# Performance work log

Hardware: AMD Instinct MI355X
Metric: run time of the kernel (lower is better)

Reference implementation:

```python
import jax, jax.numpy as jnp
import numpy as np

N = 50000      # num nodes
E = 600000     # num edges (avg degree 12)
IN = 256       # in_feats
H = 128        # h_feats
P = 2          # prop_step
LN_EPS = 1e-5


def setup_inputs() -> dict:
    key = jax.random.key(0)
    ks = jax.random.split(key, 8)
    return {
        "in_feat": jax.random.normal(ks[0], (N, IN), jnp.float32),
        "row": jax.random.randint(ks[1], (E,), 0, N),  # target node of each edge
        "col": jax.random.randint(ks[2], (E,), 0, N),  # source node of each edge
        "lin_w": jax.random.normal(ks[3], (H, IN), jnp.float32) / np.sqrt(IN).astype(np.float32),
        "lin_b": jnp.zeros((H,), jnp.float32),
        "conv_w": jax.random.normal(ks[4], (H, H), jnp.float32) / np.sqrt(H).astype(np.float32),
        "conv_b": jnp.zeros((H,), jnp.float32),
        "root_emb": jax.random.normal(ks[5], (1, H), jnp.float32) * 0.02,
        "ln_gamma": jnp.ones((P, H), jnp.float32),
        "ln_beta": jnp.zeros((P, H), jnp.float32),
    }


def _layernorm(x, g, b):
    mu = jnp.mean(x, axis=-1, keepdims=True)
    var = jnp.mean(jnp.square(x - mu), axis=-1, keepdims=True)
    return (x - mu) * jax.lax.rsqrt(var + LN_EPS) * g + b


def reference(in_feat, row, col, lin_w, lin_b, conv_w, conv_b, root_emb, ln_gamma, ln_beta):
    n = in_feat.shape[0]
    h = in_feat @ lin_w.T + lin_b                      # [N, H]

    # OGB-style degree norm with +1 trick (original edges, row = target)
    deg = jax.ops.segment_sum(jnp.ones_like(row, dtype=h.dtype), row, num_segments=n) + 1.0
    deg_inv = 1.0 / deg                                # deg >= 1, never inf

    # GCNConv symmetric norm with self loops: D^-1/2 (A+I) D^-1/2
    loop = jnp.arange(n)
    r2 = jnp.concatenate([row, loop])                  # [E+N] targets
    c2 = jnp.concatenate([col, loop])                  # [E+N] sources
    d2 = jax.ops.segment_sum(jnp.ones_like(r2, dtype=h.dtype), r2, num_segments=n)
    dis = jnp.where(d2 > 0, jax.lax.rsqrt(jnp.maximum(d2, 1.0)), 0.0)
    ew = dis[r2] * dis[c2]                             # [E+N] edge weights

    root = root_emb[0]                                 # [H]
    ori = h
    for i in range(P):
        if i != 0:
            h = h + ori                                # residual
            h = _layernorm(h, ln_gamma[i], ln_beta[i])
            h = jax.nn.relu(h)
            # dropout=0.0 -> identity
        xw = h @ conv_w.T                              # [N, H]
        h_msg = jax.ops.segment_sum(ew[:, None] * xw[c2], r2, num_segments=n) + conv_b
        root_contrib = jax.nn.relu(h + root) * deg_inv[:, None]
        h = h_msg + root_contrib
    return h
```

## Files before the change

### kernel.cpp

```cpp
#include <hip/hip_runtime.h>

#define NN 50000
#define EE 600000
#define INF 256
#define HF 128
#define CEB ((EE + 255) / 256)
#define GB ((NN + 63) / 64)
#define NBCH ((NN + 255) / 256)

typedef __attribute__((ext_vector_type(8))) short short8;
typedef __attribute__((ext_vector_type(4))) float floatx4;

__device__ __forceinline__ unsigned short f32_to_bf16_rne(float x) {
    unsigned int u = __float_as_uint(x);
    unsigned int r = (u + 0x7FFFu + ((u >> 16) & 1u)) >> 16;
    return (unsigned short)r;
}
__device__ __forceinline__ float bf16_to_f32(unsigned short h) {
    return __uint_as_float(((unsigned int)h) << 16);
}
__device__ __forceinline__ float bf16lo_u32(unsigned int u) {
    return __uint_as_float(u << 16);
}
__device__ __forceinline__ float bf16hi_u32(unsigned int u) {
    return __uint_as_float(u & 0xFFFF0000u);
}
__device__ __forceinline__ void cvt_hilo8(float4 v0, float4 v1, short8& hs, short8& ls) {
    float x[8] = {v0.x, v0.y, v0.z, v0.w, v1.x, v1.y, v1.z, v1.w};
    union { short8 s; unsigned short u[8]; } H, L;
#pragma unroll
    for (int k = 0; k < 8; ++k) {
        unsigned short hi = f32_to_bf16_rne(x[k]);
        H.u[k] = hi;
        L.u[k] = f32_to_bf16_rne(x[k] - bf16_to_f32(hi));
    }
    hs = H.s;
    ls = L.s;
}

__global__ void scan_phase1(const int* __restrict__ cnt, int* __restrict__ bsum, int n) {
    __shared__ int sdata[256];
    int t = threadIdx.x;
    int i = blockIdx.x * 256 + t;
    sdata[t] = (i < n) ? cnt[i] : 0;
    __syncthreads();
    for (int s = 128; s > 0; s >>= 1) {
        if (t < s) sdata[t] += sdata[t + s];
        __syncthreads();
    }
    if (t == 0) bsum[blockIdx.x] = sdata[0];
}

__global__ void scan_phase3(const int* __restrict__ cnt, const int* __restrict__ bsum,
                            int* __restrict__ row_start,
                            float* __restrict__ deg_inv, float* __restrict__ dis,
                            int n, int nb, int E) {
    __shared__ int sb[256];
    __shared__ int sdata[256];
    int t = threadIdx.x;
    sb[t] = (t < nb) ? bsum[t] : 0;
    __syncthreads();
    for (int s = 1; s < 256; s <<= 1) {
        int add = (t >= s) ? sb[t - s] : 0;
        __syncthreads();
        sb[t] += add;
        __syncthreads();
    }
    int base = sb[blockIdx.x] - bsum[blockIdx.x];
    int i = blockIdx.x * 256 + t;
    int v = (i < n) ? cnt[i] : 0;
    sdata[t] = v;
    __syncthreads();
    for (int s = 1; s < 256; s <<= 1) {
        int add = (t >= s) ? sdata[t - s] : 0;
        __syncthreads();
        sdata[t] += add;
        __syncthreads();
    }
    if (i < n) {
        row_start[i] = base + sdata[t] - v;
        float d = (float)(v + 1);
        deg_inv[i] = 1.0f / d;
        dis[i] = rsqrtf(d);
    }
    if (blockIdx.x == 0 && t == 0) row_start[n] = E;
}

__global__ void fill_csr(const int* __restrict__ row, const int* __restrict__ col,
                         const int* __restrict__ row_start, const int* __restrict__ pos,
                         int* __restrict__ csr_col, int E) {
    int e = blockIdx.x * blockDim.x + threadIdx.x;
    if (e < E) {
        int p = row_start[row[e]] + pos[e];
        __builtin_nontemporal_store(col[e], &csr_col[p]);
    }
}

template <int K, int MODE>
__device__ __forceinline__ void gemm_tile(
    int bidx,
    const float* __restrict__ Af,
    const unsigned short* __restrict__ Ahg, const unsigned short* __restrict__ Alg,
    const float* __restrict__ Wsrc,
    const float* __restrict__ bias,
    float* __restrict__ C, unsigned short* __restrict__ Cbf,
    const float* __restrict__ h, const float* __restrict__ deg_inv,
    const float* __restrict__ root,
    const float* __restrict__ gamma, const float* __restrict__ beta,
    unsigned short* WS, int M) {
    constexpr int NKC = K / 32;
    const int t = threadIdx.x;
    const int wave = t >> 6;
    const int lane = t & 63;
    const int lrow = lane & 15;
    const int quad = lane >> 4;
    const int bm = bidx * 64;
    int arow = bm + wave * 16 + lrow;
    if (arow >= M) arow = M - 1;

    floatx4 acc[8];
#pragma unroll
    for (int nt = 0; nt < 8; ++nt) acc[nt] = (floatx4){0.f, 0.f, 0.f, 0.f};

#pragma unroll
    for (int pp = 0; pp < NKC / 2; ++pp) {
        if (pp) __syncthreads();
#pragma unroll
        for (int u0 = 0; u0 < 4; ++u0) {
            int u = t + u0 * 256;
            int kc2 = u >> 9;
            int nt = (u >> 6) & 7;
            int ln = u & 63;
            int rw = nt * 16 + (ln & 15);
            int koff = (pp * 2 + kc2) * 32 + (ln >> 4) * 8;
            const float* p = &Wsrc[(size_t)rw * K + koff];
            float4 v0 = *reinterpret_cast<const float4*>(p);
            float4 v1 = *reinterpret_cast<const float4*>(p + 4);
            short8 hs, ls;
            cvt_hilo8(v0, v1, hs, ls);
            *reinterpret_cast<short8*>(&WS[kc2 * 8192 + nt * 512 + ln * 8]) = hs;
            *reinterpret_cast<short8*>(&WS[kc2 * 8192 + 4096 + nt * 512 + ln * 8]) = ls;
        }
        __syncthreads();
#pragma unroll
        for (int k2 = 0; k2 < 2; ++k2) {
            int kc = pp * 2 + k2;
            short8 afh, afl;
            if (MODE == 0) {
                const float* ap = &Af[(size_t)arow * K + kc * 32 + quad * 8];
                float4 a0 = *reinterpret_cast<const float4*>(ap);
                float4 a1 = *reinterpret_cast<const float4*>(ap + 4);
                cvt_hilo8(a0, a1, afh, afl);
            } else {
                size_t ao = (size_t)arow * K + kc * 32 + quad * 8;
                afh = *reinterpret_cast<const short8*>(&Ahg[ao]);
                afl = *reinterpret_cast<const short8*>(&Alg[ao]);
            }
            const unsigned short* wb = &WS[k2 * 8192 + lane * 8];
#pragma unroll
            for (int nt = 0; nt < 8; ++nt) {
                short8 bfh = *reinterpret_cast<const short8*>(wb + nt * 512);
                short8 bfl = *reinterpret_cast<const short8*>(wb + 4096 + nt * 512);
                acc[nt] = __builtin_amdgcn_mfma_f32_16x16x32_bf16(afh, bfh, acc[nt], 0, 0, 0);
                acc[nt] = __builtin_amdgcn_mfma_f32_16x16x32_bf16(afl, bfh, acc[nt], 0, 0, 0);
                acc[nt] = __builtin_amdgcn_mfma_f32_16x16x32_bf16(afh, bfl, acc[nt], 0, 0, 0);
            }
        }
    }

    float cb[8], rt[8], gm[8], bt[8];
#pragma unroll
    for (int nt = 0; nt < 8; ++nt) {
        int colh = nt * 16 + lrow;
        cb[nt] = bias[colh];
        if (MODE >= 1) rt[nt] = root[colh];
        if (MODE == 1) { gm[nt] = gamma[colh]; bt[nt] = beta[colh]; }
    }

#pragma unroll
    for (int r = 0; r < 4; ++r) {
        int grow = bm + wave * 16 + quad * 4 + r;
        bool ok = (grow < M);
        int gr = ok ? grow : M - 1;
        float x[8];
        if (MODE == 0) {
#pragma unroll
            for (int nt = 0; nt < 8; ++nt) x[nt] = acc[nt][r] + cb[nt];
        } else {
            float di = deg_inv[gr];
            float hv[8];
#pragma unroll
            for (int nt = 0; nt < 8; ++nt) hv[nt] = h[(size_t)gr * HF + nt * 16 + lrow];
#pragma unroll
            for (int nt = 0; nt < 8; ++nt) {
                float v = acc[nt][r] + cb[nt] + fmaxf(hv[nt] + rt[nt], 0.f) * di;
                x[nt] = (MODE == 1) ? v + hv[nt] : v;
            }
        }
        if (MODE == 1) {
            float s = 0.f;
#pragma unroll
            for (int nt = 0; nt < 8; ++nt) s += x[nt];
#pragma unroll
            for (int m = 1; m < 16; m <<= 1) s += __shfl_xor(s, m, 64);
            float mu = s * (1.0f / HF);
            float var = 0.f;
#pragma unroll
            for (int nt = 0; nt < 8; ++nt) { float d = x[nt] - mu; var += d * d; }
#pragma unroll
            for (int m = 1; m < 16; m <<= 1) var += __shfl_xor(var, m, 64);
            float rs = rsqrtf(var * (1.0f / HF) + 1e-5f);
            if (ok) {
#pragma unroll
                for (int nt = 0; nt < 8; ++nt) {
                    int colh = nt * 16 + lrow;
                    float y = fmaxf((x[nt] - mu) * rs * gm[nt] + bt[nt], 0.f);
                    C[(size_t)grow * HF + colh] = y;
                    Cbf[(size_t)grow * HF + colh] = f32_to_bf16_rne(y);
                }
            }
        } else if (MODE == 0) {
            if (ok) {
#pragma unroll
                for (int nt = 0; nt < 8; ++nt) {
                    int colh = nt * 16 + lrow;
                    C[(size_t)grow * HF + colh] = x[nt];
                    Cbf[(size_t)grow * HF + colh] = f32_to_bf16_rne(x[nt]);
                }
            }
        } else {
            if (ok) {
#pragma unroll
                for (int nt = 0; nt < 8; ++nt)
                    C[(size_t)grow * HF + nt * 16 + lrow] = x[nt];
            }
        }
    }
}

__global__ __launch_bounds__(256) void gemm0_count(
    const float* __restrict__ in_feat, const float* __restrict__ lin_w,
    const float* __restrict__ lin_b,
    float* __restrict__ h0, unsigned short* __restrict__ hbf,
    const int* __restrict__ row, int* __restrict__ cnt, int* __restrict__ pos) {
    __shared__ unsigned short WS[2 * 8192];
    int b = blockIdx.x;
    if (b < GB) {
        gemm_tile<INF, 0>(b, in_feat, nullptr, nullptr, lin_w, lin_b,
                          h0, hbf, nullptr, nullptr, nullptr,
                          nullptr, nullptr, WS, NN);
        return;
    }
    int e = (b - GB) * 256 + threadIdx.x;
    if (e < EE) pos[e] = atomicAdd(&cnt[row[e]], 1);
}

template <int MODE>
__global__ __launch_bounds__(256) void gemm_conv(
    const unsigned short* __restrict__ agg_hi, const unsigned short* __restrict__ agg_lo,
    const float* __restrict__ conv_w, const float* __restrict__ conv_b,
    float* __restrict__ C, unsigned short* __restrict__ Cbf,
    const float* __restrict__ h, const float* __restrict__ deg_inv,
    const float* __restrict__ root,
    const float* __restrict__ gamma, const float* __restrict__ beta) {
    __shared__ unsigned short WS[2 * 8192];
    gemm_tile<HF, MODE>(blockIdx.x, nullptr, agg_hi, agg_lo, conv_w, conv_b,
                        C, Cbf, h, deg_inv, root, gamma, beta, WS, NN);
}

__global__ void aggregate(const int* __restrict__ row_start, const int* __restrict__ csr_col,
                          const float* __restrict__ dis, const float* __restrict__ deg_inv,
                          const float* __restrict__ h, const unsigned short* __restrict__ hbf,
                          unsigned short* __restrict__ agg_hi, unsigned short* __restrict__ agg_lo,
                          int n) {
    int wid = (blockIdx.x * blockDim.x + threadIdx.x) >> 6;
    int lane = threadIdx.x & 63;
    if (wid >= n) return;
    int q = lane >> 4;
    int l16 = lane & 15;
    int s = row_start[wid];
    int e = row_start[wid + 1];
    float a0 = 0.f, a1 = 0.f, a2 = 0.f, a3 = 0.f, a4 = 0.f, a5 = 0.f, a6 = 0.f, a7 = 0.f;
    if (e - s <= 16) {
        int j0 = s + q;
        bool p0 = j0 < e, p1 = j0 + 4 < e, p2 = j0 + 8 < e, p3 = j0 + 12 < e;
        int c0 = p0 ? csr_col[j0] : 0;
        int c1 = p1 ? csr_col[j0 + 4] : 0;
        int c2 = p2 ? csr_col[j0 + 8] : 0;
        int c3 = p3 ? csr_col[j0 + 12] : 0;
        float d0 = dis[c0], d1 = dis[c1], d2 = dis[c2], d3 = dis[c3];
        uint4 z = make_uint4(0, 0, 0, 0);
        uint4 g0 = z, g1 = z, g2 = z, g3 = z;
        if (p0) g0 = *reinterpret_cast<const uint4*>(&hbf[(size_t)c0 * HF + l16 * 8]);
        if (p1) g1 = *reinterpret_cast<const uint4*>(&hbf[(size_t)c1 * HF + l16 * 8]);
        if (p2) g2 = *reinterpret_cast<const uint4*>(&hbf[(size_t)c2 * HF + l16 * 8]);
        if (p3) g3 = *reinterpret_cast<const uint4*>(&hbf[(size_t)c3 * HF + l16 * 8]);
        a0 = d0 * bf16lo_u32(g0.x) + d1 * bf16lo_u32(g1.x) + d2 * bf16lo_u32(g2.x) + d3 * bf16lo_u32(g3.x);
        a1 = d0 * bf16hi_u32(g0.x) + d1 * bf16hi_u32(g1.x) + d2 * bf16hi_u32(g2.x) + d3 * bf16hi_u32(g3.x);
        a2 = d0 * bf16lo_u32(g0.y) + d1 * bf16lo_u32(g1.y) + d2 * bf16lo_u32(g2.y) + d3 * bf16lo_u32(g3.y);
        a3 = d0 * bf16hi_u32(g0.y) + d1 * bf16hi_u32(g1.y) + d2 * bf16hi_u32(g2.y) + d3 * bf16hi_u32(g3.y);
        a4 = d0 * bf16lo_u32(g0.z) + d1 * bf16lo_u32(g1.z) + d2 * bf16lo_u32(g2.z) + d3 * bf16lo_u32(g3.z);
        a5 = d0 * bf16hi_u32(g0.z) + d1 * bf16hi_u32(g1.z) + d2 * bf16hi_u32(g2.z) + d3 * bf16hi_u32(g3.z);
        a6 = d0 * bf16lo_u32(g0.w) + d1 * bf16lo_u32(g1.w) + d2 * bf16lo_u32(g2.w) + d3 * bf16lo_u32(g3.w);
        a7 = d0 * bf16hi_u32(g0.w) + d1 * bf16hi_u32(g1.w) + d2 * bf16hi_u32(g2.w) + d3 * bf16hi_u32(g3.w);
    } else {
        float b0 = 0.f, b1 = 0.f, b2 = 0.f, b3 = 0.f, b4 = 0.f, b5 = 0.f, b6 = 0.f, b7 = 0.f;
        int j = s + q;
        for (; j + 4 < e; j += 8) {
            int c0 = csr_col[j];
            int c1 = csr_col[j + 4];
            float d0 = dis[c0];
            float d1 = dis[c1];
            uint4 h0 = *reinterpret_cast<const uint4*>(&hbf[(size_t)c0 * HF + l16 * 8]);
            uint4 h1 = *reinterpret_cast<const uint4*>(&hbf[(size_t)c1 * HF + l16 * 8]);
            a0 = fmaf(d0, bf16lo_u32(h0.x), a0); a1 = fmaf(d0, bf16hi_u32(h0.x), a1);
            a2 = fmaf(d0, bf16lo_u32(h0.y), a2); a3 = fmaf(d0, bf16hi_u32(h0.y), a3);
            a4 = fmaf(d0, bf16lo_u32(h0.z), a4); a5 = fmaf(d0, bf16hi_u32(h0.z), a5);
            a6 = fmaf(d0, bf16lo_u32(h0.w), a6); a7 = fmaf(d0, bf16hi_u32(h0.w), a7);
            b0 = fmaf(d1, bf16lo_u32(h1.x), b0); b1 = fmaf(d1, bf16hi_u32(h1.x), b1);
            b2 = fmaf(d1, bf16lo_u32(h1.y), b2); b3 = fmaf(d1, bf16hi_u32(h1.y), b3);
            b4 = fmaf(d1, bf16lo_u32(h1.z), b4); b5 = fmaf(d1, bf16hi_u32(h1.z), b5);
            b6 = fmaf(d1, bf16lo_u32(h1.w), b6); b7 = fmaf(d1, bf16hi_u32(h1.w), b7);
        }
        if (j < e) {
            int c0 = csr_col[j];
            float d0 = dis[c0];
            uint4 h0 = *reinterpret_cast<const uint4*>(&hbf[(size_t)c0 * HF + l16 * 8]);
            a0 = fmaf(d0, bf16lo_u32(h0.x), a0); a1 = fmaf(d0, bf16hi_u32(h0.x), a1);
            a2 = fmaf(d0, bf16lo_u32(h0.y), a2); a3 = fmaf(d0, bf16hi_u32(h0.y), a3);
            a4 = fmaf(d0, bf16lo_u32(h0.z), a4); a5 = fmaf(d0, bf16hi_u32(h0.z), a5);
            a6 = fmaf(d0, bf16lo_u32(h0.w), a6); a7 = fmaf(d0, bf16hi_u32(h0.w), a7);
        }
        a0 += b0; a1 += b1; a2 += b2; a3 += b3;
        a4 += b4; a5 += b5; a6 += b6; a7 += b7;
    }
#pragma unroll
    for (int m = 16; m < 64; m <<= 1) {
        a0 += __shfl_xor(a0, m, 64);
        a1 += __shfl_xor(a1, m, 64);
        a2 += __shfl_xor(a2, m, 64);
        a3 += __shfl_xor(a3, m, 64);
        a4 += __shfl_xor(a4, m, 64);
        a5 += __shfl_xor(a5, m, 64);
        a6 += __shfl_xor(a6, m, 64);
        a7 += __shfl_xor(a7, m, 64);
    }
    if (q == 0) {
        float dn = dis[wid];
        float di = deg_inv[wid];
        float4 hA = *reinterpret_cast<const float4*>(&h[(size_t)wid * HF + l16 * 8]);
        float4 hB = *reinterpret_cast<const float4*>(&h[(size_t)wid * HF + l16 * 8 + 4]);
        float o[8];
        o[0] = fmaf(dn, a0, di * hA.x);
        o[1] = fmaf(dn, a1, di * hA.y);
        o[2] = fmaf(dn, a2, di * hA.z);
        o[3] = fmaf(dn, a3, di * hA.w);
        o[4] = fmaf(dn, a4, di * hB.x);
        o[5] = fmaf(dn, a5, di * hB.y);
        o[6] = fmaf(dn, a6, di * hB.z);
        o[7] = fmaf(dn, a7, di * hB.w);
        unsigned short hi[8], lo[8];
#pragma unroll
        for (int k = 0; k < 8; ++k) {
            hi[k] = f32_to_bf16_rne(o[k]);
            lo[k] = f32_to_bf16_rne(o[k] - bf16_to_f32(hi[k]));
        }
        uint4 hp, lp;
        hp.x = (unsigned)hi[0] | ((unsigned)hi[1] << 16);
        hp.y = (unsigned)hi[2] | ((unsigned)hi[3] << 16);
        hp.z = (unsigned)hi[4] | ((unsigned)hi[5] << 16);
        hp.w = (unsigned)hi[6] | ((unsigned)hi[7] << 16);
        lp.x = (unsigned)lo[0] | ((unsigned)lo[1] << 16);
        lp.y = (unsigned)lo[2] | ((unsigned)lo[3] << 16);
        lp.z = (unsigned)lo[4] | ((unsigned)lo[5] << 16);
        lp.w = (unsigned)lo[6] | ((unsigned)lo[7] << 16);
        *reinterpret_cast<uint4*>(&agg_hi[(size_t)wid * HF + l16 * 8]) = hp;
        *reinterpret_cast<uint4*>(&agg_lo[(size_t)wid * HF + l16 * 8]) = lp;
    }
}

extern "C" void kernel_launch(void* const* d_in, const int* in_sizes, int n_in,
                              void* d_out, int out_size, void* d_ws, size_t ws_size,
                              hipStream_t stream) {
    const int N = NN, E = EE;
    const float* in_feat = (const float*)d_in[0];
    const int* row = (const int*)d_in[1];
    const int* col = (const int*)d_in[2];
    const float* lin_w = (const float*)d_in[3];
    const float* lin_b = (const float*)d_in[4];
    const float* conv_w = (const float*)d_in[5];
    const float* conv_b = (const float*)d_in[6];
    const float* root_emb = (const float*)d_in[7];
    const float* ln_gamma = (const float*)d_in[8];
    const float* ln_beta = (const float*)d_in[9];
    float* out = (float*)d_out;

    float* ws = (float*)d_ws;
    size_t o = 0;
    float* deg_inv = ws + o; o += N;
    float* dis = ws + o; o += N;
    int* cnt = (int*)(ws + o); o += N;
    int* row_start = (int*)(ws + o); o += N + 4;
    int* pos = (int*)(ws + o); o += E;
    int* bsum = (int*)(ws + o); o += 256;
    int* csr_col = (int*)(ws + o); o += E;
    float* h0 = ws + o; o += (size_t)N * HF;
    unsigned short* hbf = (unsigned short*)(ws + o); o += (size_t)N * HF / 2;
    unsigned short* agg_hi = (unsigned short*)(ws + o); o += (size_t)N * HF / 2;
    unsigned short* agg_lo = (unsigned short*)(ws + o); o += (size_t)N * HF / 2;

    const int WB = (N + 3) / 4;

    hipMemsetAsync(cnt, 0, N * sizeof(int), stream);

    gemm0_count<<<GB + CEB, 256, 0, stream>>>(in_feat, lin_w, lin_b, h0, hbf,
                                              row, cnt, pos);
    scan_phase1<<<NBCH, 256, 0, stream>>>(cnt, bsum, N);
    scan_phase3<<<NBCH, 256, 0, stream>>>(cnt, bsum, row_start, deg_inv, dis, N, NBCH, E);
    fill_csr<<<CEB, 256, 0, stream>>>(row, col, row_start, pos, csr_col, E);

    aggregate<<<WB, 256, 0, stream>>>(row_start, csr_col, dis, deg_inv, h0, hbf,
                                      agg_hi, agg_lo, N);
    gemm_conv<1><<<GB, 256, 0, stream>>>(agg_hi, agg_lo, conv_w, conv_b, h0, hbf,
                                         h0, deg_inv, root_emb,
                                         ln_gamma + HF, ln_beta + HF);

    aggregate<<<WB, 256, 0, stream>>>(row_start, csr_col, dis, deg_inv, h0, hbf,
                                      agg_hi, agg_lo, N);
    gemm_conv<2><<<GB, 256, 0, stream>>>(agg_hi, agg_lo, conv_w, conv_b, out, nullptr,
                                         h0, deg_inv, root_emb, nullptr, nullptr);
}
```

Baseline: 285.5 us.

## Prepack bf16 hi/lo weights once, merge scan kernels, split GEMM0 across CSR phases

A new prologue kernel converts lin_w and conv_w once into the MFMA-ready bf16 hi/lo fragment layout and zeroes the degree counters, replacing the memset. GEMM tiles then copy the prepacked weights straight into LDS (via global_load_lds when available) instead of reconverting them from fp32 in every block. The two scan kernels become one, with a last-block-done atomic finishing the cross-block offsets. The first linear GEMM is split so some tiles run beside the edge counting and the rest run beside the CSR fill, removing a launch and overlapping work. The risks are the extra prologue launch, the single-block serial fixup pass over row_start, and relying on the threadfence/atomic ordering being correct.

```diff
diff --git a/kernel.cpp b/kernel.cpp
--- a/kernel.cpp
+++ b/kernel.cpp
@@ -1,11 +1,14 @@
 #include <hip/hip_runtime.h>
+#include <stdint.h>
 
 #define NN 50000
 #define EE 600000
 #define INF 256
 #define HF 128
 #define CEB ((EE + 255) / 256)
-#define GB ((NN + 63) / 64)
+#define GBT ((NN + 63) / 64)
+#define NT0 500
+#define NT1 (GBT - NT0)
 #define NBCH ((NN + 255) / 256)
 
 typedef __attribute__((ext_vector_type(8))) short short8;
@@ -38,37 +41,43 @@
     ls = L.s;
 }
 
-__global__ void scan_phase1(const int* __restrict__ cnt, int* __restrict__ bsum, int n) {
+__device__ __forceinline__ void prepack_one(int idx, const float* lw, const float* cw,
+                                            unsigned short* fl, unsigned short* fc) {
+    const float* src; unsigned short* dst; int K, c;
+    if (idx < 8192) { src = lw; dst = fl; K = INF; c = idx; }
+    else            { src = cw; dst = fc; K = HF; c = idx - 8192; }
+    int lane = c & 63;
+    int nt = (c >> 6) & 7;
+    int hl = (c >> 9) & 1;
+    int kc = c >> 10;
+    int rw = nt * 16 + (lane & 15);
+    int koff = kc * 32 + (lane >> 4) * 8;
+    const float* p = &src[(size_t)rw * K + koff];
+    float4 v0 = *reinterpret_cast<const float4*>(p);
+    float4 v1 = *reinterpret_cast<const float4*>(p + 4);
+    short8 hs, ls;
+    cvt_hilo8(v0, v1, hs, ls);
+    *reinterpret_cast<short8*>(&dst[(size_t)c * 8]) = hl ? ls : hs;
+}
+
+__global__ void zero_prepack(const float* __restrict__ lw, const float* __restrict__ cw,
+                             unsigned short* __restrict__ fl, unsigned short* __restrict__ fc,
+                             int* __restrict__ cnt, int* __restrict__ done_ctr) {
+    int g = blockIdx.x * 256 + threadIdx.x;
+    if (g < 12288) prepack_one(g, lw, cw, fl, fc);
+    for (int i = g; i < NN; i += 256 * 256) cnt[i] = 0;
+    if (g == 0) *done_ctr = 0;
+}
+
+__global__ void scan_all(const int* __restrict__ cnt, int* __restrict__ bsum,
+                         int* __restrict__ done_ctr, int* __restrict__ row_start,
+                         float* __restrict__ deg_inv, float* __restrict__ dis) {
     __shared__ int sdata[256];
-    int t = threadIdx.x;
-    int i = blockIdx.x * 256 + t;
-    sdata[t] = (i < n) ? cnt[i] : 0;
-    __syncthreads();
-    for (int s = 128; s > 0; s >>= 1) {
-        if (t < s) sdata[t] += sdata[t + s];
-        __syncthreads();
-    }
-    if (t == 0) bsum[blockIdx.x] = sdata[0];
-}
-
-__global__ void scan_phase3(const int* __restrict__ cnt, const int* __restrict__ bsum,
-                            int* __restrict__ row_start,
-                            float* __restrict__ deg_inv, float* __restrict__ dis,
-                            int n, int nb, int E) {
-    __shared__ int sb[256];
-    __shared__ int sdata[256];
-    int t = threadIdx.x;
-    sb[t] = (t < nb) ? bsum[t] : 0;
-    __syncthreads();
-    for (int s = 1; s < 256; s <<= 1) {
-        int add = (t >= s) ? sb[t - s] : 0;
-        __syncthreads();
-        sb[t] += add;
-        __syncthreads();
-    }
-    int base = sb[blockIdx.x] - bsum[blockIdx.x];
-    int i = blockIdx.x * 256 + t;
-    int v = (i < n) ? cnt[i] : 0;
+    __shared__ int eb[256];
+    __shared__ int flag;
+    int c = blockIdx.x, t = threadIdx.x;
+    int i = c * 256 + t;
+    int v = (i < NN) ? cnt[i] : 0;
     sdata[t] = v;
     __syncthreads();
     for (int s = 1; s < 256; s <<= 1) {
@@ -77,23 +86,34 @@
         sdata[t] += add;
         __syncthreads();
     }
-    if (i < n) {
-        row_start[i] = base + sdata[t] - v;
+    if (i < NN) {
+        row_start[i] = sdata[t] - v;
         float d = (float)(v + 1);
         deg_inv[i] = 1.0f / d;
         dis[i] = rsqrtf(d);
     }
-    if (blockIdx.x == 0 && t == 0) row_start[n] = E;
-}
-
-__global__ void fill_csr(const int* __restrict__ row, const int* __restrict__ col,
-                         const int* __restrict__ row_start, const int* __restrict__ pos,
-                         int* __restrict__ csr_col, int E) {
-    int e = blockIdx.x * blockDim.x + threadIdx.x;
-    if (e < E) {
-        int p = row_start[row[e]] + pos[e];
-        __builtin_nontemporal_store(col[e], &csr_col[p]);
-    }
+    if (t == 255) bsum[c] = sdata[255];
+    __syncthreads();
+    if (t == 0) {
+        __threadfence();
+        flag = (atomicAdd(done_ctr, 1) == NBCH - 1);
+    }
+    __syncthreads();
+    if (!flag) return;
+    __threadfence();
+    int bv = (t < NBCH) ? bsum[t] : 0;
+    sdata[t] = bv;
+    __syncthreads();
+    for (int s = 1; s < 256; s <<= 1) {
+        int add = (t >= s) ? sdata[t - s] : 0;
+        __syncthreads();
+        sdata[t] += add;
+        __syncthreads();
+    }
+    eb[t] = sdata[t] - bv;
+    __syncthreads();
+    for (int j = t; j < NN; j += 256) row_start[j] += eb[j >> 8];
+    if (t == 0) row_start[NN] = EE;
 }
 
 template <int K, int MODE>
@@ -101,7 +121,7 @@
     int bidx,
     const float* __restrict__ Af,
     const unsigned short* __restrict__ Ahg, const unsigned short* __restrict__ Alg,
-    const float* __restrict__ Wsrc,
+    const unsigned short* __restrict__ Wf,
     const float* __restrict__ bias,
     float* __restrict__ C, unsigned short* __restrict__ Cbf,
     const float* __restrict__ h, const float* __restrict__ deg_inv,
@@ -125,21 +145,22 @@
 #pragma unroll
     for (int pp = 0; pp < NKC / 2; ++pp) {
         if (pp) __syncthreads();
-#pragma unroll
-        for (int u0 = 0; u0 < 4; ++u0) {
-            int u = t + u0 * 256;
-            int kc2 = u >> 9;
-            int nt = (u >> 6) & 7;
-            int ln = u & 63;
-            int rw = nt * 16 + (ln & 15);
-            int koff = (pp * 2 + kc2) * 32 + (ln >> 4) * 8;
-            const float* p = &Wsrc[(size_t)rw * K + koff];
-            float4 v0 = *reinterpret_cast<const float4*>(p);
-            float4 v1 = *reinterpret_cast<const float4*>(p + 4);
-            short8 hs, ls;
-            cvt_hilo8(v0, v1, hs, ls);
-            *reinterpret_cast<short8*>(&WS[kc2 * 8192 + nt * 512 + ln * 8]) = hs;
-            *reinterpret_cast<short8*>(&WS[kc2 * 8192 + 4096 + nt * 512 + ln * 8]) = ls;
+        {
+            const unsigned short* src = Wf + (size_t)pp * 16384 + (size_t)t * 8;
+#if __has_builtin(__builtin_amdgcn_global_load_lds)
+#pragma unroll
+            for (int i = 0; i < 8; ++i) {
+                __builtin_amdgcn_global_load_lds(
+                    (const unsigned int*)(src + (size_t)i * 2048),
+                    (unsigned int*)(WS + ((size_t)i * 256 + (t >> 6) * 64) * 8),
+                    16, 0, 0);
+            }
+#else
+            const uint4* s4 = reinterpret_cast<const uint4*>(Wf + (size_t)pp * 16384);
+            uint4* d4 = reinterpret_cast<uint4*>(WS);
+#pragma unroll
+            for (int i = 0; i < 8; ++i) d4[t + 256 * i] = s4[t + 256 * i];
+#endif
         }
         __syncthreads();
 #pragma unroll
@@ -239,32 +260,54 @@
 }
 
 __global__ __launch_bounds__(256) void gemm0_count(
-    const float* __restrict__ in_feat, const float* __restrict__ lin_w,
+    const float* __restrict__ in_feat, const unsigned short* __restrict__ fl,
     const float* __restrict__ lin_b,
     float* __restrict__ h0, unsigned short* __restrict__ hbf,
     const int* __restrict__ row, int* __restrict__ cnt, int* __restrict__ pos) {
     __shared__ unsigned short WS[2 * 8192];
     int b = blockIdx.x;
-    if (b < GB) {
-        gemm_tile<INF, 0>(b, in_feat, nullptr, nullptr, lin_w, lin_b,
+    if (b < NT0) {
+        gemm_tile<INF, 0>(b, in_feat, nullptr, nullptr, fl, lin_b,
                           h0, hbf, nullptr, nullptr, nullptr,
                           nullptr, nullptr, WS, NN);
         return;
     }
-    int e = (b - GB) * 256 + threadIdx.x;
+    int e = (b - NT0) * 256 + threadIdx.x;
     if (e < EE) pos[e] = atomicAdd(&cnt[row[e]], 1);
+}
+
+__global__ __launch_bounds__(256) void gemm0_fill(
+    const float* __restrict__ in_feat, const unsigned short* __restrict__ fl,
+    const float* __restrict__ lin_b,
+    float* __restrict__ h0, unsigned short* __restrict__ hbf,
+    const int* __restrict__ row, const int* __restrict__ col,
+    const int* __restrict__ row_start, const int* __restrict__ pos,
+    int* __restrict__ csr_col) {
+    __shared__ unsigned short WS[2 * 8192];
+    int b = blockIdx.x;
+    if (b < NT1) {
+        gemm_tile<INF, 0>(NT0 + b, in_feat, nullptr, nullptr, fl, lin_b,
+                          h0, hbf, nullptr, nullptr, nullptr,
+                          nullptr, nullptr, WS, NN);
+        return;
+    }
+    int e = (b - NT1) * 256 + threadIdx.x;
+    if (e < EE) {
+        int p = row_start[row[e]] + pos[e];
+        __builtin_nontemporal_store(col[e], &csr_col[p]);
+    }
 }
 
 template <int MODE>
 __global__ __launch_bounds__(256) void gemm_conv(
     const unsigned short* __restrict__ agg_hi, const unsigned short* __restrict__ agg_lo,
-    const float* __restrict__ conv_w, const float* __restrict__ conv_b,
+    const unsigned short* __restrict__ fc, const float* __restrict__ conv_b,
     float* __restrict__ C, unsigned short* __restrict__ Cbf,
     const float* __restrict__ h, const float* __restrict__ deg_inv,
     const float* __restrict__ root,
     const float* __restrict__ gamma, const float* __restrict__ beta) {
     __shared__ unsigned short WS[2 * 8192];
-    gemm_tile<HF, MODE>(blockIdx.x, nullptr, agg_hi, agg_lo, conv_w, conv_b,
+    gemm_tile<HF, MODE>(blockIdx.x, nullptr, agg_hi, agg_lo, fc, conv_b,
                         C, Cbf, h, deg_inv, root, gamma, beta, WS, NN);
 }
 
@@ -382,7 +425,7 @@
 extern "C" void kernel_launch(void* const* d_in, const int* in_sizes, int n_in,
                               void* d_out, int out_size, void* d_ws, size_t ws_size,
                               hipStream_t stream) {
-    const int N = NN, E = EE;
+    const int N = NN;
     const float* in_feat = (const float*)d_in[0];
     const int* row = (const int*)d_in[1];
     const int* col = (const int*)d_in[2];
@@ -401,9 +444,12 @@
     float* dis = ws + o; o += N;
     int* cnt = (int*)(ws + o); o += N;
     int* row_start = (int*)(ws + o); o += N + 4;
-    int* pos = (int*)(ws + o); o += E;
+    int* pos = (int*)(ws + o); o += EE;
     int* bsum = (int*)(ws + o); o += 256;
-    int* csr_col = (int*)(ws + o); o += E;
+    int* done_ctr = (int*)(ws + o); o += 4;
+    int* csr_col = (int*)(ws + o); o += EE;
+    unsigned short* fl = (unsigned short*)(ws + o); o += 32768;
+    unsigned short* fc = (unsigned short*)(ws + o); o += 16384;
     float* h0 = ws + o; o += (size_t)N * HF;
     unsigned short* hbf = (unsigned short*)(ws + o); o += (size_t)N * HF / 2;
     unsigned short* agg_hi = (unsigned short*)(ws + o); o += (size_t)N * HF / 2;
@@ -411,22 +457,20 @@
 
     const int WB = (N + 3) / 4;
 
-    hipMemsetAsync(cnt, 0, N * sizeof(int), stream);
-
-    gemm0_count<<<GB + CEB, 256, 0, stream>>>(in_feat, lin_w, lin_b, h0, hbf,
-                                              row, cnt, pos);
-    scan_phase1<<<NBCH, 256, 0, stream>>>(cnt, bsum, N);
-    scan_phase3<<<NBCH, 256, 0, stream>>>(cnt, bsum, row_start, deg_inv, dis, N, NBCH, E);
-    fill_csr<<<CEB, 256, 0, stream>>>(row, col, row_start, pos, csr_col, E);
+    zero_prepack<<<256, 256, 0, stream>>>(lin_w, conv_w, fl, fc, cnt, done_ctr);
+    gemm0_count<<<NT0 + CEB, 256, 0, stream>>>(in_feat, fl, lin_b, h0, hbf, row, cnt, pos);
+    scan_all<<<NBCH, 256, 0, stream>>>(cnt, bsum, done_ctr, row_start, deg_inv, dis);
+    gemm0_fill<<<NT1 + CEB, 256, 0, stream>>>(in_feat, fl, lin_b, h0, hbf,
+                                              row, col, row_start, pos, csr_col);
 
     aggregate<<<WB, 256, 0, stream>>>(row_start, csr_col, dis, deg_inv, h0, hbf,
                                       agg_hi, agg_lo, N);
-    gemm_conv<1><<<GB, 256, 0, stream>>>(agg_hi, agg_lo, conv_w, conv_b, h0, hbf,
-                                         h0, deg_inv, root_emb,
-                                         ln_gamma + HF, ln_beta + HF);
+    gemm_conv<1><<<GBT, 256, 0, stream>>>(agg_hi, agg_lo, fc, conv_b, h0, hbf,
+                                          h0, deg_inv, root_emb,
+                                          ln_gamma + HF, ln_beta + HF);
 
     aggregate<<<WB, 256, 0, stream>>>(row_start, csr_col, dis, deg_inv, h0, hbf,
                                       agg_hi, agg_lo, N);
-    gemm_conv<2><<<GB, 256, 0, stream>>>(agg_hi, agg_lo, conv_w, conv_b, out, nullptr,
-                                         h0, deg_inv, root_emb, nullptr, nullptr);
-}
+    gemm_conv<2><<<GBT, 256, 0, stream>>>(agg_hi, agg_lo, fc, conv_b, out, nullptr,
+                                          h0, deg_inv, root_emb, nullptr, nullptr);
+}
```

Result: slower. 308.9 us (+8.2%).
